# Kernel optimization log

Measured on AMD Instinct MI355X. Metric: run time of the kernel, lower is better.

The kernel has to match this reference:

```python
import jax, jax.numpy as jnp
import numpy as np

# module hyperparameters (match init_kwargs)
D_IN = 32
N_BAND_IN = 32
D_OUT = 32
K_BAND = 4
K_T = 3
DIL_T = 1
STRIDE_B = 2
PAD_B = 1
PAD_B_OUT = 0

# derived band geometry (same formulas as ConvTranspose2dBandPadder)
N_UP = (N_BAND_IN - 1) * STRIDE_B + 1            # zero-interleaved bands
PAD_TOP = K_BAND - 1 - PAD_B
PAD_BOT = PAD_TOP + PAD_B_OUT
N_PADDED = N_UP + PAD_TOP + PAD_BOT              # bands fed to the conv
N_BAND_OUT = N_PADDED - K_BAND + 1               # valid conv along bands

B = 8
T = 1000


def setup_inputs() -> dict:
    key = jax.random.key(0)
    k1, k2, k3 = jax.random.split(key, 3)
    x = jax.random.normal(k1, (B, D_IN * N_BAND_IN, T), jnp.float32)
    W = jax.random.normal(k2, (D_OUT, D_IN, K_BAND, K_T), jnp.float32) * 0.05
    b = jax.random.normal(k3, (D_OUT,), jnp.float32) * 0.05
    return {"x": x, "W": W, "b": b}


def reference(x, W, b):
    """x: (B, D_IN*N_BAND_IN, T) band-major channels -> (B, D_OUT*N_BAND_OUT, T)."""
    Bs, _, Ts = x.shape
    # chunk(dim=1, n_band_in): band-major layout (band, feature)
    bands = x.reshape(Bs, N_BAND_IN, D_IN, Ts)
    # zero-interleave bands by stride + top/bottom zero-band padding
    up = jnp.zeros((Bs, N_PADDED, D_IN, Ts), x.dtype)
    up = up.at[:, PAD_TOP:PAD_TOP + N_UP:STRIDE_B].set(bands)
    # 2D conv: channels = D_IN, spatial = (band, time), causal in time
    xin = up.transpose(0, 2, 1, 3)  # (B, D_IN, N_PADDED, T)
    pad_t = (K_T - 1) * DIL_T
    y = jax.lax.conv_general_dilated(
        xin, W,
        window_strides=(1, 1),
        padding=((0, 0), (pad_t, 0)),  # valid over bands, causal over time
        rhs_dilation=(1, DIL_T),
        dimension_numbers=("NCHW", "OIHW", "NCHW"),
    )  # (B, D_OUT, N_BAND_OUT, T)
    y = y + b[None, :, None, None]
    # back to band-major flattened channels
    return y.transpose(0, 2, 1, 3).reshape(Bs, D_OUT * N_BAND_OUT, Ts)
```

## Files before the change

kernel.cpp:

```cpp
#include <hip/hip_runtime.h>
#include <cstddef>
#include <cstdint>


typedef __bf16 bf16x8 __attribute__((ext_vector_type(8)));
typedef __bf16 bf16x4 __attribute__((ext_vector_type(4)));
typedef float  f32x4  __attribute__((ext_vector_type(4)));

#define D_IN_ 32
#define D_OUT_ 32
#define N_BI_ 32
#define N_BO_ 64
#define K_B_ 4
#define K_T_ 3
#define T_ 1000
#define B_ 8

#define TT_ 500
#define XR_ 512
#define ROWB_ 64
#define WT_ELEMS (2 * 6 * 2 * 64 * 8)

__device__ __forceinline__ int swz(int t) { return (t & 3) ^ ((t >> 2) & 3); }

__global__ __launch_bounds__(256)
void wprep(const float* __restrict__ W, __bf16* __restrict__ wt) {
    int idx = blockIdx.x * 256 + threadIdx.x;
    if (idx >= WT_ELEMS) return;
    int r = idx & 7, l = (idx >> 3) & 63, mt = (idx >> 9) & 1, rest = idx >> 10;
    int ks = rest % 6, p = rest / 6;
    int dout = mt * 16 + (l & 15), din = (l >> 4) * 8 + r;
    int j = ks / 3, kt = ks % 3, kb = 2 * j + p;
    wt[idx] = (__bf16)W[((dout * D_IN_ + din) * K_B_ + kb) * K_T_ + kt];
}

__global__ __launch_bounds__(512, 2)
void tct_pair(const float* __restrict__ x, const __bf16* __restrict__ wt,
              const float* __restrict__ bias, float* __restrict__ out)
{
    __shared__ unsigned char xl[2 * XR_ * ROWB_];

    const int wg  = blockIdx.x;
    const int bb  = wg & 7;
    const int rr  = wg >> 3;
    const int kk  = rr >> 1;
    const int th  = rr & 1;
    const int k   = kk - 1;
    const int t0  = th * TT_;

    const int tid = threadIdx.x;
    const int l   = tid & 63;
    const int w   = tid >> 6;
    const int mt  = w >> 2;
    const int wq  = w & 3;
    const int tl  = l & 15;
    const int cch = l >> 4;

    {
        const int g  = tid >> 4;
        const int u  = tid & 15;
        const int si = u >> 3;
        const int dg = u & 7;
        const int s  = k + si;
        const bool bandok = (s >= 0) && (s < N_BI_);
        const float* xb = x + ((size_t)(bb * N_BI_ + (bandok ? s : 0)) * D_IN_ + dg * 4) * T_;
        unsigned char* lbase = xl + si * (XR_ * ROWB_);
        const int c = dg >> 1, h = dg & 1;

        f32x4 vv[4][4];
#pragma unroll
        for (int it = 0; it < 4; ++it) {
            const int tg = t0 - 4 + (g + it * 32) * 4;
            const bool ok = bandok && (tg >= 0) && (tg < T_);
#pragma unroll
            for (int i = 0; i < 4; ++i)
                vv[it][i] = ok ? *(const f32x4*)(xb + (size_t)i * T_ + tg)
                               : (f32x4){0.f, 0.f, 0.f, 0.f};
        }
#pragma unroll
        for (int it = 0; it < 4; ++it) {
            const int tq = g + it * 32;
#pragma unroll
            for (int e = 0; e < 4; ++e) {
                const int t = tq * 4 + e;
                bf16x4 row;
                row[0] = (__bf16)vv[it][0][e];
                row[1] = (__bf16)vv[it][1][e];
                row[2] = (__bf16)vv[it][2][e];
                row[3] = (__bf16)vv[it][3][e];
                *(bf16x4*)(lbase + t * ROWB_ + ((c ^ swz(t)) << 4) + (h << 3)) = row;
            }
        }
    }

    bf16x8 afrag[2][6];
    {
        const bf16x8* wp = (const bf16x8*)wt;
#pragma unroll
        for (int p = 0; p < 2; ++p)
#pragma unroll
            for (int ks = 0; ks < 6; ++ks)
                afrag[p][ks] = wp[p * 768 + ks * 128 + mt * 64 + l];
    }

    const int rbase = cch * 4;
    float bv[4];
#pragma unroll
    for (int r = 0; r < 4; ++r) bv[r] = bias[mt * 16 + rbase + r];

    __syncthreads();

#pragma unroll
    for (int ntc = 0; ntc < 2; ++ntc) {
        f32x4 acc[2][4];
#pragma unroll
        for (int p = 0; p < 2; ++p)
#pragma unroll
            for (int n4 = 0; n4 < 4; ++n4)
#pragma unroll
                for (int r = 0; r < 4; ++r) acc[p][n4][r] = 0.f;

#pragma unroll
        for (int n4 = 0; n4 < 4; ++n4) {
            const int nt = ntc * 4 + n4;
#pragma unroll
            for (int j = 0; j < 2; ++j) {
                const unsigned char* xbnd = xl + j * (XR_ * ROWB_);
#pragma unroll
                for (int kt = 0; kt < 3; ++kt) {
                    const int lt = (wq * 128 + nt * 16 + tl + kt + 2) & (XR_ - 1);
                    const bf16x8 bfrag = *(const bf16x8*)(xbnd + lt * ROWB_
                                                          + ((cch ^ swz(lt)) << 4));
                    const int ks = j * 3 + kt;
                    acc[0][n4] = __builtin_amdgcn_mfma_f32_16x16x32_bf16(afrag[0][ks], bfrag, acc[0][n4], 0, 0, 0);
                    acc[1][n4] = __builtin_amdgcn_mfma_f32_16x16x32_bf16(afrag[1][ks], bfrag, acc[1][n4], 0, 0, 0);
                }
            }
        }

#pragma unroll
        for (int p = 0; p < 2; ++p) {
            const int n = 2 * k + 2 - p;
            if (n < 0 || n >= N_BO_) continue;
            float* opb = out + ((size_t)(bb * N_BO_ + n) * D_OUT_ + mt * 16 + rbase) * T_;
#pragma unroll
            for (int n4 = 0; n4 < 4; ++n4) {
                const int lcol = wq * 128 + (ntc * 4 + n4) * 16 + tl;
                if (lcol < TT_) {
                    const int tcol = t0 + lcol;
#pragma unroll
                    for (int r = 0; r < 4; ++r)
                        opb[(size_t)r * T_ + tcol] = acc[p][n4][r] + bv[r];
                }
            }
        }
    }
}

__global__ __launch_bounds__(256)
void tct_fallback(const float* __restrict__ x, const float* __restrict__ W,
                  const float* __restrict__ bias, float* __restrict__ out)
{
    const int lane = threadIdx.x & 63;
    const int wav  = __builtin_amdgcn_readfirstlane(threadIdx.x >> 6);
    const int dog  = wav * 8;
    const int n    = blockIdx.y;
    const int bb   = blockIdx.z;
    const int p    = n & 1;
    int t0 = blockIdx.x * 256 + lane * 4;
    const bool act = (t0 < T_);
    if (!act) t0 = T_ - 4;
    float acc[8][4];
#pragma unroll
    for (int i = 0; i < 8; ++i)
#pragma unroll
        for (int u = 0; u < 4; ++u) acc[i][u] = 0.f;
#pragma unroll
    for (int j = 0; j < 2; ++j) {
        const int s = (n + 2 * j + p - 2) >> 1;
        if (s < 0 || s >= N_BI_) continue;
        const int kb = 2 * j + p;
        const float* xband = x + (size_t)(bb * N_BI_ + s) * D_IN_ * T_;
        for (int d_in = 0; d_in < D_IN_; ++d_in) {
            const float* xr = xband + d_in * T_;
            const float4 xc = *(const float4*)(xr + t0);
            float4 xp = make_float4(0.f, 0.f, 0.f, 0.f);
            if (t0 > 0) xp = *(const float4*)(xr + t0 - 4);
            const float xv[6] = {xp.z, xp.w, xc.x, xc.y, xc.z, xc.w};
#pragma unroll
            for (int kt = 0; kt < K_T_; ++kt) {
                float wv[8];
#pragma unroll
                for (int i = 0; i < 8; ++i) {
                    const int widx = __builtin_amdgcn_readfirstlane(
                        (((dog + i) * D_IN_ + d_in) * K_B_ + kb) * K_T_ + kt);
                    wv[i] = W[widx];
                }
#pragma unroll
                for (int i = 0; i < 8; ++i)
#pragma unroll
                    for (int u = 0; u < 4; ++u)
                        acc[i][u] = fmaf(wv[i], xv[u + kt], acc[i][u]);
            }
        }
    }
    if (act) {
        float bvv[8];
#pragma unroll
        for (int i = 0; i < 8; ++i) bvv[i] = bias[dog + i];
        float* op = out + ((size_t)(bb * N_BO_ + n) * D_OUT_ + dog) * T_ + t0;
#pragma unroll
        for (int i = 0; i < 8; ++i) {
            float4 v;
            v.x = acc[i][0] + bvv[i]; v.y = acc[i][1] + bvv[i];
            v.z = acc[i][2] + bvv[i]; v.w = acc[i][3] + bvv[i];
            *(float4*)(op + (size_t)i * T_) = v;
        }
    }
}

extern "C" void kernel_launch(void* const* d_in, const int* in_sizes, int n_in,
                              void* d_out, int out_size, void* d_ws, size_t ws_size,
                              hipStream_t stream) {
    const float* x    = (const float*)d_in[0];
    const float* W    = (const float*)d_in[1];
    const float* bias = (const float*)d_in[2];
    float* out = (float*)d_out;

    if (ws_size >= (size_t)WT_ELEMS * sizeof(__bf16)) {
        __bf16* wt = (__bf16*)d_ws;
        wprep<<<(WT_ELEMS + 255) / 256, 256, 0, stream>>>(W, wt);
        tct_pair<<<dim3(8 * 33 * 2), dim3(512), 0, stream>>>(x, wt, bias, out);
    } else {
        tct_fallback<<<dim3((T_ + 255) / 256, N_BO_, B_), dim3(256), 0, stream>>>(x, W, bias, out);
    }
}
```

Before: 106.1 us.

## Split time tile into two double-buffered sub-tiles overlapping loads with MFMA compute

Each workgroup's 500-column time tile is now processed as two LDS sub-tiles of 256 rows. The loads for the second sub-tile are issued while the first sub-tile is being computed, so global-to-LDS staging overlaps with MFMA work. Total LDS stays the same, but fewer registers are held at once, and the launch bound now asks for 4 workgroups per CU instead of 2 to raise occupancy. In exchange there are 4 halo columns of redundant loads per sub-tile, an extra barrier, and a risk of register spills under the tighter bound.

After: 110.3 us. 1.04x slower.

```diff
diff --git a/kernel.cpp b/kernel.cpp
--- a/kernel.cpp
+++ b/kernel.cpp
@@ -16,9 +16,9 @@
 #define T_ 1000
 #define B_ 8
 
-#define TT_ 500
-#define XR_ 512
-#define ROWB_ 64
+#define XRS_ 256
+#define BANDSTR_ (XRS_ * 64)
+#define SUBSTR_ (2 * BANDSTR_)
 #define WT_ELEMS (2 * 6 * 2 * 64 * 8)
 
 __device__ __forceinline__ int swz(int t) { return (t & 3) ^ ((t >> 2) & 3); }
@@ -34,11 +34,79 @@
     wt[idx] = (__bf16)W[((dout * D_IN_ + din) * K_B_ + kb) * K_T_ + kt];
 }
 
-__global__ __launch_bounds__(512, 2)
+__device__ __forceinline__ void stage_load(const float* xb, bool bandok,
+                                           int tbase, int g, int it, f32x4 vv[4]) {
+    const int tg = tbase + (g + it * 32) * 4;
+    const bool ok = bandok && (tg >= 0) && (tg < T_);
+#pragma unroll
+    for (int i = 0; i < 4; ++i)
+        vv[i] = ok ? *(const f32x4*)(xb + (size_t)i * T_ + tg)
+                   : (f32x4){0.f, 0.f, 0.f, 0.f};
+}
+
+__device__ __forceinline__ void stage_write(unsigned char* lbase, int c, int h,
+                                            int g, int it, const f32x4 vv[4]) {
+#pragma unroll
+    for (int e = 0; e < 4; ++e) {
+        const int r = (g + it * 32) * 4 + e;
+        bf16x4 row;
+        row[0] = (__bf16)vv[0][e];
+        row[1] = (__bf16)vv[1][e];
+        row[2] = (__bf16)vv[2][e];
+        row[3] = (__bf16)vv[3][e];
+        *(bf16x4*)(lbase + r * 64 + ((c ^ swz(r)) << 4) + (h << 3)) = row;
+    }
+}
+
+__device__ __forceinline__ void compute_half(
+    const unsigned char* xls, const bf16x8 afrag[2][6], const float bv[4],
+    int wq, int tl, int cch, int nth, int k, int bb, int mt, int rbase,
+    int sub, int t0, float* __restrict__ out)
+{
+#pragma unroll
+    for (int n4 = 0; n4 < 2; ++n4) {
+        const int nt = nth * 2 + n4;
+        const int lcol = wq * 64 + nt * 16 + tl;
+        f32x4 acc[2];
+#pragma unroll
+        for (int p = 0; p < 2; ++p)
+#pragma unroll
+            for (int r = 0; r < 4; ++r) acc[p][r] = 0.f;
+
+#pragma unroll
+        for (int j = 0; j < 2; ++j) {
+            const unsigned char* xbnd = xls + j * BANDSTR_;
+#pragma unroll
+            for (int kt = 0; kt < 3; ++kt) {
+                const int lt = (lcol + kt + 2) & (XRS_ - 1);
+                const bf16x8 bfrag = *(const bf16x8*)(xbnd + lt * 64
+                                                      + ((cch ^ swz(lt)) << 4));
+                const int ks = j * 3 + kt;
+                acc[0] = __builtin_amdgcn_mfma_f32_16x16x32_bf16(afrag[0][ks], bfrag, acc[0], 0, 0, 0);
+                acc[1] = __builtin_amdgcn_mfma_f32_16x16x32_bf16(afrag[1][ks], bfrag, acc[1], 0, 0, 0);
+            }
+        }
+        const int cap = sub ? 248 : 252;
+        if (lcol < cap) {
+            const int tcol = t0 + sub * 252 + lcol;
+#pragma unroll
+            for (int p = 0; p < 2; ++p) {
+                const int n = 2 * k + 2 - p;
+                if (n < 0 || n >= N_BO_) continue;
+                float* opb = out + ((size_t)(bb * N_BO_ + n) * D_OUT_ + mt * 16 + rbase) * T_ + tcol;
+#pragma unroll
+                for (int r = 0; r < 4; ++r)
+                    opb[(size_t)r * T_] = acc[p][r] + bv[r];
+            }
+        }
+    }
+}
+
+__global__ __launch_bounds__(512, 4)
 void tct_pair(const float* __restrict__ x, const __bf16* __restrict__ wt,
               const float* __restrict__ bias, float* __restrict__ out)
 {
-    __shared__ unsigned char xl[2 * XR_ * ROWB_];
+    __shared__ unsigned char xl[2 * SUBSTR_];
 
     const int wg  = blockIdx.x;
     const int bb  = wg & 7;
@@ -46,7 +114,7 @@
     const int kk  = rr >> 1;
     const int th  = rr & 1;
     const int k   = kk - 1;
-    const int t0  = th * TT_;
+    const int t0  = th * 500;
 
     const int tid = threadIdx.x;
     const int l   = tid & 63;
@@ -56,42 +124,20 @@
     const int tl  = l & 15;
     const int cch = l >> 4;
 
-    {
-        const int g  = tid >> 4;
-        const int u  = tid & 15;
-        const int si = u >> 3;
-        const int dg = u & 7;
-        const int s  = k + si;
-        const bool bandok = (s >= 0) && (s < N_BI_);
-        const float* xb = x + ((size_t)(bb * N_BI_ + (bandok ? s : 0)) * D_IN_ + dg * 4) * T_;
-        unsigned char* lbase = xl + si * (XR_ * ROWB_);
-        const int c = dg >> 1, h = dg & 1;
-
-        f32x4 vv[4][4];
-#pragma unroll
-        for (int it = 0; it < 4; ++it) {
-            const int tg = t0 - 4 + (g + it * 32) * 4;
-            const bool ok = bandok && (tg >= 0) && (tg < T_);
-#pragma unroll
-            for (int i = 0; i < 4; ++i)
-                vv[it][i] = ok ? *(const f32x4*)(xb + (size_t)i * T_ + tg)
-                               : (f32x4){0.f, 0.f, 0.f, 0.f};
-        }
-#pragma unroll
-        for (int it = 0; it < 4; ++it) {
-            const int tq = g + it * 32;
-#pragma unroll
-            for (int e = 0; e < 4; ++e) {
-                const int t = tq * 4 + e;
-                bf16x4 row;
-                row[0] = (__bf16)vv[it][0][e];
-                row[1] = (__bf16)vv[it][1][e];
-                row[2] = (__bf16)vv[it][2][e];
-                row[3] = (__bf16)vv[it][3][e];
-                *(bf16x4*)(lbase + t * ROWB_ + ((c ^ swz(t)) << 4) + (h << 3)) = row;
-            }
-        }
-    }
+    const int g  = tid >> 4;
+    const int u  = tid & 15;
+    const int si = u >> 3;
+    const int dg = u & 7;
+    const int s  = k + si;
+    const bool bandok = (s >= 0) && (s < N_BI_);
+    const float* xb = x + ((size_t)(bb * N_BI_ + (bandok ? s : 0)) * D_IN_ + dg * 4) * T_;
+    unsigned char* lb0 = xl + si * BANDSTR_;
+    unsigned char* lb1 = xl + SUBSTR_ + si * BANDSTR_;
+    const int c = dg >> 1, h = dg & 1;
+
+    f32x4 vv0[4], vv1[4];
+    stage_load(xb, bandok, t0 - 4, g, 0, vv0);
+    stage_load(xb, bandok, t0 - 4, g, 1, vv1);
 
     bf16x8 afrag[2][6];
     {
@@ -102,59 +148,25 @@
             for (int ks = 0; ks < 6; ++ks)
                 afrag[p][ks] = wp[p * 768 + ks * 128 + mt * 64 + l];
     }
-
     const int rbase = cch * 4;
     float bv[4];
 #pragma unroll
     for (int r = 0; r < 4; ++r) bv[r] = bias[mt * 16 + rbase + r];
 
+    stage_write(lb0, c, h, g, 0, vv0);
+    stage_write(lb0, c, h, g, 1, vv1);
     __syncthreads();
 
-#pragma unroll
-    for (int ntc = 0; ntc < 2; ++ntc) {
-        f32x4 acc[2][4];
-#pragma unroll
-        for (int p = 0; p < 2; ++p)
-#pragma unroll
-            for (int n4 = 0; n4 < 4; ++n4)
-#pragma unroll
-                for (int r = 0; r < 4; ++r) acc[p][n4][r] = 0.f;
-
-#pragma unroll
-        for (int n4 = 0; n4 < 4; ++n4) {
-            const int nt = ntc * 4 + n4;
-#pragma unroll
-            for (int j = 0; j < 2; ++j) {
-                const unsigned char* xbnd = xl + j * (XR_ * ROWB_);
-#pragma unroll
-                for (int kt = 0; kt < 3; ++kt) {
-                    const int lt = (wq * 128 + nt * 16 + tl + kt + 2) & (XR_ - 1);
-                    const bf16x8 bfrag = *(const bf16x8*)(xbnd + lt * ROWB_
-                                                          + ((cch ^ swz(lt)) << 4));
-                    const int ks = j * 3 + kt;
-                    acc[0][n4] = __builtin_amdgcn_mfma_f32_16x16x32_bf16(afrag[0][ks], bfrag, acc[0][n4], 0, 0, 0);
-                    acc[1][n4] = __builtin_amdgcn_mfma_f32_16x16x32_bf16(afrag[1][ks], bfrag, acc[1][n4], 0, 0, 0);
-                }
-            }
-        }
-
-#pragma unroll
-        for (int p = 0; p < 2; ++p) {
-            const int n = 2 * k + 2 - p;
-            if (n < 0 || n >= N_BO_) continue;
-            float* opb = out + ((size_t)(bb * N_BO_ + n) * D_OUT_ + mt * 16 + rbase) * T_;
-#pragma unroll
-            for (int n4 = 0; n4 < 4; ++n4) {
-                const int lcol = wq * 128 + (ntc * 4 + n4) * 16 + tl;
-                if (lcol < TT_) {
-                    const int tcol = t0 + lcol;
-#pragma unroll
-                    for (int r = 0; r < 4; ++r)
-                        opb[(size_t)r * T_ + tcol] = acc[p][n4][r] + bv[r];
-                }
-            }
-        }
-    }
+    stage_load(xb, bandok, t0 + 248, g, 0, vv0);
+    compute_half(xl, afrag, bv, wq, tl, cch, 0, k, bb, mt, rbase, 0, t0, out);
+    stage_write(lb1, c, h, g, 0, vv0);
+    stage_load(xb, bandok, t0 + 248, g, 1, vv1);
+    compute_half(xl, afrag, bv, wq, tl, cch, 1, k, bb, mt, rbase, 0, t0, out);
+    stage_write(lb1, c, h, g, 1, vv1);
+    __syncthreads();
+
+    compute_half(xl + SUBSTR_, afrag, bv, wq, tl, cch, 0, k, bb, mt, rbase, 1, t0, out);
+    compute_half(xl + SUBSTR_, afrag, bv, wq, tl, cch, 1, k, bb, mt, rbase, 1, t0, out);
 }
 
 __global__ __launch_bounds__(256)
```
